# Kernel optimization log

Hardware: AMD Instinct MI355X
Metric: run time of the kernel (lower is better)

The kernel has to match this reference:

```python
import jax, jax.numpy as jnp
import numpy as np

B, N, H, D, F = 32, 128, 256, 256, 512   # batch, nodes, gru hidden, latent dim, mlp hidden
SUP = 0.5                                 # ancestor_suppression_strength
EPS = 1e-6


def _gru(x, h, Wx, Wh, bx, bh):
    """torch.nn.GRUCell math; x,h: [..., H]."""
    gx = x @ Wx + bx
    gh = h @ Wh + bh
    rx, ux, nx = jnp.split(gx, 3, axis=-1)
    rh, uh, nh = jnp.split(gh, 3, axis=-1)
    r = jax.nn.sigmoid(rx + rh)
    u = jax.nn.sigmoid(ux + uh)
    n = jnp.tanh(nx + r * nh)
    return (1.0 - u) * n + u * h


def setup_inputs() -> dict:
    key = jax.random.key(0)
    ks = jax.random.split(key, 12)
    rn = lambda k, shape, fan: jax.random.normal(k, shape, jnp.float32) * (fan ** -0.5)
    return {
        "z": jax.random.normal(ks[0], (B, D), jnp.float32),
        "targets": jax.random.randint(ks[1], (B, N, N), 0, 2, jnp.int32),
        "W_init": rn(ks[2], (D, H), D),
        "b_init": jnp.zeros((H,), jnp.float32),
        "Wx": rn(ks[3], (H, 3 * H), H),
        "Wh": rn(ks[4], (H, 3 * H), H),
        "bx": jnp.zeros((3 * H,), jnp.float32),
        "bh": jnp.zeros((3 * H,), jnp.float32),
        "W1": rn(ks[5], (2 * H + D, F), 2 * H + D),
        "b1": jnp.zeros((F,), jnp.float32),
        "W2": rn(ks[6], (F, 1), F),
        "b2": jnp.zeros((1,), jnp.float32),
    }


def reference(z, targets, W_init, b_init, Wx, Wh, bx, bh, W1, b1, W2, b2):
    # teacher-forcing link targets: strictly lower-triangular (parents have smaller index)
    tgt = jnp.tril(targets.astype(jnp.float32), k=-1)  # [B,N,N]
    idx = jnp.arange(N)

    def decode_one(z1, t1):  # z1:[D], t1:[N,N]
        h0 = jnp.tanh(z1 @ W_init + b_init)                      # decoder_init: z -> node-0 state
        states0 = jnp.zeros((N, H), jnp.float32).at[0].set(h0)
        A0 = jnp.zeros((N, N), jnp.float32)                      # ancestor bitset: A[i,j]=1 iff j ancestor of i

        def step(carry, t):
            states, A, ll = carry
            m = (idx < t).astype(jnp.float32)                    # existing-node mask
            pooled = (states * m[:, None]).sum(0) / m.sum()      # mean aggregation
            h_prov = _gru(pooled, h0, Wx, Wh, bx, bh)            # provisional new-node state
            # parent logits: MLP([h_new, h_j, z]) for every existing node j
            feat = jnp.concatenate([jnp.broadcast_to(h_prov, (N, H)), states,
                                    jnp.broadcast_to(z1, (N, D))], axis=-1)   # [N, 2H+D]
            logits = (jax.nn.relu(feat @ W1 + b1) @ W2 + b2)[:, 0]            # [N]
            row = t1[t]                                          # teacher-forced parents of node t
            anc = jnp.minimum(row @ A, 1.0)                      # j already ancestor of a chosen parent
            q = jnp.clip(jax.nn.sigmoid(logits) * (1.0 - SUP * anc), EPS, 1.0 - EPS)
            ll = ll + (m * (row * jnp.log(q) + (1.0 - row) * jnp.log1p(-q))).sum()
            A = A.at[t].set(jnp.minimum(row + row @ A, 1.0))     # ancestors(t) = parents U their ancestors
            states = states.at[t].set(h_prov)
            m2 = (idx <= t).astype(jnp.float32)[:, None]
            pooled2 = (states * m2).sum(0) / m2.sum()
            upd = _gru(jnp.broadcast_to(pooled2, (N, H)), states, Wx, Wh, bx, bh)
            states = m2 * upd + (1.0 - m2) * states              # propagate info among generated nodes
            return (states, A, ll), None

        (states, A, ll), _ = jax.lax.scan(step, (states0, A0, jnp.zeros((), jnp.float32)),
                                          jnp.arange(1, N))
        return t1, ll                                            # link matrix (teacher forced), log-likelihood

    L, ll = jax.vmap(decode_one)(z, tgt)
    return L, ll
```

## Files before the change

kernel.cpp:

```cpp
#include <hip/hip_runtime.h>
#include <hip/hip_bf16.h>
#include <math.h>

#define Bz 32
#define Nn 128
#define Hh 256
#define Dd 256
#define Ff 512
#define Gg 768
#define NT 512

typedef short v8s __attribute__((ext_vector_type(8)));
typedef float f4  __attribute__((ext_vector_type(4)));
#define MFMA(a,b,c) __builtin_amdgcn_mfma_f32_16x16x32_bf16(a,b,c,0,0,0)

#define WS_H0    0
#define WS_GH0   (WS_H0 + Bz*Hh)
#define WS_ZW1   (WS_GH0 + Bz*Gg)
#define WS_GXP   (WS_ZW1 + Bz*Ff)
#define WS_LOGP  (WS_GXP + Bz*2*8*Gg)
#define WS_BAR   (WS_LOGP + Bz*2*8*Nn)
#define WS_XS    (WS_BAR + Bz*32)
#define WS_WB    (WS_XS + Bz*32768)

#define SM_SW    0
#define SM_SST   81920
#define SM_NLDS  147456
#define SM_GXF   155648
#define SM_HPF   158720
#define SM_GX2   159232
#define SM_GHT   159616
#define SM_BASE  160000
#define SM_BHS   160256
#define SM_PSN   160640
#define SM_LOGI  160768
#define SM_TGR   161280
#define SM_RBIT  161536
#define SM_ANCW  161568
#define SM_AMASK 161600
#define SMEM_SZ  163648

__device__ __forceinline__ unsigned short f2bf(float x) {
  unsigned u = __float_as_uint(x);
  u = u + 0x7fffu + ((u >> 16) & 1u);
  return (unsigned short)(u >> 16);
}
__device__ __forceinline__ unsigned pack2(float e, float o) {
  return (unsigned)f2bf(e) | ((unsigned)f2bf(o) << 16);
}
__device__ __forceinline__ unsigned pkbf(float x, float y) {
  __hip_bfloat162 h = __float22bfloat162_rn(make_float2(x, y));
  union { __hip_bfloat162 h; unsigned u; } c; c.h = h; return c.u;
}
__device__ __forceinline__ float bf2f(unsigned short s) {
  return __uint_as_float(((unsigned)s) << 16);
}
__device__ __forceinline__ float sigm(float x) { return 1.0f / (1.0f + __expf(-x)); }
__device__ __forceinline__ float tanh_fast(float x) { return 2.0f / (1.0f + __expf(-2.0f*x)) - 1.0f; }
__device__ __forceinline__ v8s u4v(uint4 q) { union { uint4 q; v8s v; } c; c.q = q; return c.v; }

__device__ __forceinline__ void ast32(unsigned* p, unsigned v) {
  __hip_atomic_store(p, v, __ATOMIC_RELAXED, __HIP_MEMORY_SCOPE_AGENT);
}
__device__ __forceinline__ unsigned ald32(const unsigned* p) {
  return __hip_atomic_load(p, __ATOMIC_RELAXED, __HIP_MEMORY_SCOPE_AGENT);
}
__device__ __forceinline__ void ast64(unsigned long long* p, unsigned long long v) {
  __hip_atomic_store(p, v, __ATOMIC_RELAXED, __HIP_MEMORY_SCOPE_AGENT);
}
__device__ __forceinline__ unsigned long long ald64(const unsigned long long* p) {
  return __hip_atomic_load(p, __ATOMIC_RELAXED, __HIP_MEMORY_SCOPE_AGENT);
}

__device__ __forceinline__ void waitflags(const unsigned* FLG, int lane, int r, unsigned tgt)
{
  const bool watch = (lane < 8) && (lane != r);
  for (;;) {
    const unsigned f = watch ? ald32(FLG + lane) : 0xFFFFFFFFu;
    if (__ballot(f >= tgt) == 0xFFFFFFFFFFFFFFFFull) break;
  }
  __atomic_signal_fence(__ATOMIC_ACQUIRE);
}

__global__ void __launch_bounds__(256) prep_init(
    const int* __restrict__ tg, const float* __restrict__ Wx,
    const float* __restrict__ Wh, const float* __restrict__ W1,
    float* __restrict__ ws, float* __restrict__ out)
{
  const int stride = gridDim.x * blockDim.x;
  const int t0 = blockIdx.x * blockDim.x + threadIdx.x;

  for (int i = t0; i < Bz*Nn*Nn; i += stride) {
    int col = i & (Nn-1), row = (i >> 7) & (Nn-1);
    out[i] = (col < row) ? (float)tg[i] : 0.0f;
  }
  for (int i = t0; i < Bz; i += stride) out[Bz*Nn*Nn + i] = 0.0f;

  unsigned* BARu = (unsigned*)(ws + WS_BAR);
  for (int i = t0; i < Bz*32; i += stride) BARu[i] = 0u;

  unsigned* Wb = (unsigned*)(ws + WS_WB);
  for (int i = t0; i < 160*2048; i += stride) {
    int jw = i & 3, l = (i >> 2) & 63, ks = (i >> 8) & 7, nt = i >> 11;
    int k = ks*32 + (l >> 4)*8 + 2*jw;
    int n16 = l & 15;
    float lo, hi;
    if (nt < 48)       { int c = nt*16 + n16;        lo = Wh[k*Gg + c];      hi = Wh[(k+1)*Gg + c]; }
    else if (nt < 80)  { int f = (nt-48)*16 + n16;   lo = W1[(Hh+k)*Ff + f]; hi = W1[(Hh+k+1)*Ff + f]; }
    else if (nt < 128) { int c = (nt-80)*16 + n16;   lo = Wx[k*Gg + c];      hi = Wx[(k+1)*Gg + c]; }
    else               { int f = (nt-128)*16 + n16;  lo = W1[k*Ff + f];      hi = W1[(k+1)*Ff + f]; }
    Wb[i] = pack2(lo, hi);
  }
}

__global__ void __launch_bounds__(256) prep_batch(
    const float* __restrict__ z, const float* __restrict__ Wi,
    const float* __restrict__ bi, const float* __restrict__ Wh,
    const float* __restrict__ bh, const float* __restrict__ W1,
    float* __restrict__ ws)
{
  const int b = blockIdx.x, tid = threadIdx.x;
  __shared__ float zs[Dd], h0s[Hh];
  zs[tid] = z[b*Dd + tid];
  __syncthreads();
  float acc = bi[tid];
  for (int d = 0; d < Dd; ++d) acc = fmaf(zs[d], Wi[d*Hh + tid], acc);
  const float h0 = tanhf(acc);
  h0s[tid] = h0;
  ws[WS_H0 + b*Hh + tid] = h0;
  __syncthreads();
  for (int g = tid; g < Gg; g += 256) {
    float a = bh[g];
    for (int h = 0; h < Hh; ++h) a = fmaf(h0s[h], Wh[h*Gg + g], a);
    ws[WS_GH0 + b*Gg + g] = a;
  }
  for (int f = tid; f < Ff; f += 256) {
    float a = 0.0f;
    for (int d = 0; d < Dd; ++d) a = fmaf(zs[d], W1[(2*Hh + d)*Ff + f], a);
    ws[WS_ZW1 + b*Ff + f] = a;
  }
}

__device__ __forceinline__ void G_mfma(const unsigned short* SST, const uint4* SW4,
    int mt0, bool do1, int lane, f4* acc)
{
  #pragma unroll
  for (int ks = 0; ks < 8; ++ks) {
    const v8s a0 = *(const v8s*)(SST + (mt0*8 + ks)*512 + lane*8);
    const v8s w0 = u4v(SW4[(0*8 + ks)*64 + lane]);
    const v8s w1 = u4v(SW4[(1*8 + ks)*64 + lane]);
    const v8s w2 = u4v(SW4[(2*8 + ks)*64 + lane]);
    const v8s w3 = u4v(SW4[(3*8 + ks)*64 + lane]);
    const v8s w4 = u4v(SW4[(4*8 + ks)*64 + lane]);
    const v8s w5 = u4v(SW4[(5*8 + ks)*64 + lane]);
    acc[0] = MFMA(a0,w0,acc[0]); acc[1] = MFMA(a0,w1,acc[1]);
    acc[2] = MFMA(a0,w2,acc[2]); acc[3] = MFMA(a0,w3,acc[3]);
    acc[4] = MFMA(a0,w4,acc[4]); acc[5] = MFMA(a0,w5,acc[5]);
    if (do1) {
      const v8s a1 = *(const v8s*)(SST + ((mt0+1)*8 + ks)*512 + lane*8);
      acc[6]  = MFMA(a1,w0,acc[6]);  acc[7]  = MFMA(a1,w1,acc[7]);
      acc[8]  = MFMA(a1,w2,acc[8]);  acc[9]  = MFMA(a1,w3,acc[9]);
      acc[10] = MFMA(a1,w4,acc[10]); acc[11] = MFMA(a1,w5,acc[11]);
    }
  }
}

__device__ __forceinline__ void G_epi(const f4* ac, int mt, int t, int r,
    int quad, int c16, int lane, const float* GX2, const float* BHS,
    const unsigned short* SST, unsigned short* NLDS, float* PSN)
{
  #pragma unroll
  for (int ct = 0; ct < 2; ++ct) {
    const int hcl = ct*16 + c16;
    const f4 cr = ac[0 + ct], cu = ac[2 + ct], cn = ac[4 + ct];
    const float gxr = GX2[hcl], gxu = GX2[32+hcl], gxn = GX2[64+hcl];
    const float bhr = BHS[hcl], bhu = BHS[32+hcl], bhn = BHS[64+hcl];
    float colsum = 0.0f;
    #pragma unroll
    for (int rg = 0; rg < 4; ++rg) {
      const int row = mt*16 + quad*4 + rg;
      if (row < t) {
        const int spi = ((hcl>>3)*16 + quad*4 + rg)*8 + (hcl & 7);
        const float old = bf2f(SST[(mt*8 + r)*512 + spi]);
        const float rv = sigm(gxr + cr[rg] + bhr);
        const float uv = sigm(gxu + cu[rg] + bhu);
        const float nv = tanh_fast(gxn + rv*(cn[rg] + bhn));
        const float ns = (1.0f-uv)*nv + uv*old;
        NLDS[mt*512 + spi] = f2bf(ns);
        colsum += ns;
      }
    }
    colsum += __shfl_down(colsum, 16);
    colsum += __shfl_down(colsum, 32);
    if (lane < 16) atomicAdd(&PSN[ct*16 + lane], colsum);
  }
}

__device__ __forceinline__ void L_mfma(const unsigned short* SST, const uint4* SW4,
    int mt0, bool do1, int lane, f4* acc)
{
  #pragma unroll
  for (int ks = 0; ks < 8; ++ks) {
    const v8s a0 = *(const v8s*)(SST + (mt0*8 + ks)*512 + lane*8);
    const v8s c0 = u4v(SW4[(6*8 + ks)*64 + lane]);
    const v8s c1 = u4v(SW4[(7*8 + ks)*64 + lane]);
    const v8s c2 = u4v(SW4[(8*8 + ks)*64 + lane]);
    const v8s c3 = u4v(SW4[(9*8 + ks)*64 + lane]);
    acc[0] = MFMA(a0,c0,acc[0]); acc[1] = MFMA(a0,c1,acc[1]);
    acc[2] = MFMA(a0,c2,acc[2]); acc[3] = MFMA(a0,c3,acc[3]);
    if (do1) {
      const v8s a1 = *(const v8s*)(SST + ((mt0+1)*8 + ks)*512 + lane*8);
      acc[4] = MFMA(a1,c0,acc[4]); acc[5] = MFMA(a1,c1,acc[5]);
      acc[6] = MFMA(a1,c2,acc[6]); acc[7] = MFMA(a1,c3,acc[7]);
    }
  }
}

__device__ __forceinline__ void L_epi(const f4* ac, int mt, int t,
    int quad, int c16, const float* BASE, const float* w2r, float* LOGI)
{
  #pragma unroll
  for (int rg = 0; rg < 4; ++rg) {
    float v = fmaxf(ac[0][rg] + BASE[c16],    0.0f)*w2r[0]
            + fmaxf(ac[1][rg] + BASE[16+c16], 0.0f)*w2r[1]
            + fmaxf(ac[2][rg] + BASE[32+c16], 0.0f)*w2r[2]
            + fmaxf(ac[3][rg] + BASE[48+c16], 0.0f)*w2r[3];
    v += __shfl_xor(v, 1); v += __shfl_xor(v, 2);
    v += __shfl_xor(v, 4); v += __shfl_xor(v, 8);
    const int row = mt*16 + quad*4 + rg;
    if (c16 == 0 && row < t) atomicAdd(&LOGI[row], v);
  }
}

__device__ __forceinline__ void ll_gen(int tg_, int r, int lane, float b2v,
    const unsigned* LOGPb, const unsigned* RBIT, const unsigned* ANCW,
    float* out_ll)
{
  const int pp = tg_ & 1;
  const int row = 16*r + (lane >> 2);
  float term = 0.0f;
  if (row < tg_) {
    const unsigned* Lp = LOGPb + pp*1024;
    const int rr = (lane & 3)*2;
    float s = __uint_as_float(ald32(Lp + rr*128 + row))
            + __uint_as_float(ald32(Lp + (rr+1)*128 + row));
    s += __shfl_xor(s, 1); s += __shfl_xor(s, 2);
    if ((lane & 3) == 0) {
      const int w = row >> 5;
      const float anc = (float)((ANCW[pp*4 + w] >> (row & 31)) & 1u);
      float q = sigm(b2v + s) * (1.0f - 0.5f*anc);
      q = fminf(fmaxf(q, 1e-6f), 1.0f - 1e-6f);
      const unsigned rb = (RBIT[pp*4 + w] >> (row & 31)) & 1u;
      term = rb ? logf(q) : log1pf(-q);
    }
  }
  #pragma unroll
  for (int off = 1; off < 64; off <<= 1) term += __shfl_xor(term, off);
  if (lane == 0) atomicAdd(out_ll, term);
}

__global__ void __launch_bounds__(NT) decoder_main(
    const int* __restrict__ tg,
    const float* __restrict__ bx, const float* __restrict__ bh,
    const float* __restrict__ b1, const float* __restrict__ W2,
    const float* __restrict__ b2,
    float* __restrict__ ws, float* __restrict__ out)
{
  const int blk = blockIdx.x;
  const int b = blk & 31, r = blk >> 5;
  const int tid = threadIdx.x;
  const int lane = tid & 63, wv = tid >> 6;
  const int c16 = lane & 15, quad = lane >> 4;

  extern __shared__ char smem[];
  uint4* SW4 = (uint4*)(smem + SM_SW);
  unsigned short* SST = (unsigned short*)(smem + SM_SST);
  unsigned long long* SST64 = (unsigned long long*)(smem + SM_SST);
  unsigned short* NLDS = (unsigned short*)(smem + SM_NLDS);
  unsigned* NLDSu = (unsigned*)(smem + SM_NLDS);
  unsigned long long* NLDS64 = (unsigned long long*)(smem + SM_NLDS);
  float* GXF  = (float*)(smem + SM_GXF);
  unsigned short* HPF = (unsigned short*)(smem + SM_HPF);
  float* GX2  = (float*)(smem + SM_GX2);
  float* GHT  = (float*)(smem + SM_GHT);
  float* BASE = (float*)(smem + SM_BASE);
  float* BHS  = (float*)(smem + SM_BHS);
  float* PSN  = (float*)(smem + SM_PSN);
  float* LOGI = (float*)(smem + SM_LOGI);
  unsigned char* TGRu = (unsigned char*)(smem + SM_TGR);
  unsigned* RBIT  = (unsigned*)(smem + SM_RBIT);
  unsigned* ANCW  = (unsigned*)(smem + SM_ANCW);
  unsigned* AMASK = (unsigned*)(smem + SM_AMASK);

  const float* __restrict__ h0g  = ws + WS_H0  + b*Hh;
  const float* __restrict__ gh0g = ws + WS_GH0 + b*Gg;
  const float* __restrict__ zW1g = ws + WS_ZW1 + b*Ff;
  unsigned* GXPb = (unsigned*)(ws + WS_GXP) + b*2*8*Gg;
  unsigned* LOGPb = (unsigned*)(ws + WS_LOGP) + b*2*8*Nn;
  unsigned* FLG = (unsigned*)(ws + WS_BAR) + b*32;
  unsigned long long* XS64b = (unsigned long long*)(ws + WS_XS) + b*16384;
  const uint4* WB4 = (const uint4*)(ws + WS_WB);
  float* out_ll = out + Bz*Nn*Nn + b;

  for (int i = tid; i < 16384; i += NT) ((unsigned*)SST)[i] = 0u;
  for (int i = tid; i < 4096; i += NT) NLDSu[i] = 0u;
  for (int i = tid; i < 5120; i += NT) {
    const int lt = i >> 9, q = i & 511;
    int gt;
    if (lt < 6) { const int gate = lt >> 1, tt = lt & 1; gt = gate*16 + 2*r + tt; }
    else        { gt = 48 + 4*r + (lt - 6); }
    SW4[lt*512 + q] = WB4[gt*512 + q];
  }
  for (int i = tid; i < Nn*4; i += NT) AMASK[i] = 0u;
  if (tid < 96) BHS[tid] = bh[(tid >> 5)*256 + 32*r + (tid & 31)];
  if (tid < 128) TGRu[128 + tid] = (unsigned char)tg[b*Nn*Nn + 1*Nn + tid];
  float w2r[4];
  #pragma unroll
  for (int ft = 0; ft < 4; ++ft) w2r[ft] = W2[64*r + ft*16 + c16];
  const float b2v = b2[0];
  float p_bx[3][4], p_gh[3][4], p_h0[4];
  #pragma unroll
  for (int k = 0; k < 4; ++k) {
    const int c = 4*lane + k;
    p_h0[k] = h0g[c];
    #pragma unroll
    for (int g3 = 0; g3 < 3; ++g3) {
      p_bx[g3][k] = bx[g3*256 + c];
      p_gh[g3][k] = gh0g[g3*256 + c];
    }
  }
  int colj[2]; float auxj[2];
  #pragma unroll
  for (int jj = 0; jj < 2; ++jj) {
    const int j = 2*wv + jj;
    colj[jj] = 0; auxj[jj] = 0.0f;
    if (j >= 6 && j < 12) {
      const int jx = j - 6, g = jx >> 1, tt = jx & 1;
      const int col = g*256 + 32*r + tt*16 + c16;
      colj[jj] = col; auxj[jj] = bx[col];
    } else if (j >= 12) {
      const int ft = j - 12, f = 64*r + ft*16 + c16;
      auxj[jj] = zW1g[f] + b1[f];
    }
  }
  __syncthreads();
  if (tid < Hh) {
    const int c = tid;
    SST[(c>>5)*512 + ((c>>3)&3)*128 + (c&7)] = f2bf(h0g[c]);
  }
  if (tid < 32) PSN[tid] = h0g[32*r + tid];
  __syncthreads();
  {
    union { unsigned u[4]; v8s v; } cv;
    const float4 a0 = *(const float4*)(PSN + quad*8);
    const float4 a1 = *(const float4*)(PSN + quad*8 + 4);
    cv.u[0] = pkbf(a0.x, a0.y); cv.u[1] = pkbf(a0.z, a0.w);
    cv.u[2] = pkbf(a1.x, a1.y); cv.u[3] = pkbf(a1.z, a1.w);
    const v8s avp = cv.v;
    unsigned* GXPw = GXPb + 1*8*Gg + r*Gg;
    #pragma unroll
    for (int k2 = 0; k2 < 6; ++k2) {
      const int nt = wv*6 + k2;
      f4 c = {0.0f,0.0f,0.0f,0.0f};
      c = MFMA(avp, u4v(WB4[(80 + nt)*512 + r*64 + lane]), c);
      if (quad == 0) ast32(GXPw + nt*16 + c16, __float_as_uint(c[0]));
    }
  }
  if (tid < 128) ast64(XS64b + r*128 + tid, SST64[r*128 + tid]);
  __builtin_amdgcn_s_waitcnt(0x0F70);
  __syncthreads();
  if (tid == 0) { __atomic_signal_fence(__ATOMIC_RELEASE); ast32(FLG + r, 1u); }

  for (int t = 1; t < Nn; ++t) {
    const int tp = t & 1;
    const float invt  = 1.0f / (float)t;
    const float invt1 = 1.0f / (float)(t + 1);
    const int Mr   = (t + 15) >> 4;
    const int Mtot = (t + 16) >> 4;
    const int mtc  = t >> 4;
    const int nG = (Mr + 1) >> 1, nL = (Mr + 1) >> 1;
    const int njobs = nG + nL;

    waitflags(FLG, lane, r, (unsigned)t);

    if (tid < 384) {
      const unsigned long long* GXPr = (const unsigned long long*)(GXPb + tp*8*Gg);
      unsigned long long g[8];
      #pragma unroll
      for (int rr = 0; rr < 8; ++rr) g[rr] = ald64(GXPr + rr*384 + tid);
      float s0 = 0.0f, s1 = 0.0f;
      #pragma unroll
      for (int rr = 0; rr < 8; ++rr) {
        s0 += __uint_as_float((unsigned)g[rr]);
        s1 += __uint_as_float((unsigned)(g[rr] >> 32));
      }
      GXF[2*tid]   = s0;
      GXF[2*tid+1] = s1;
    }
    if (tid < 448) {
      const unsigned long long* XSr = XS64b + ((t-1)&1)*8192;
      for (int i = tid; i < Mr*1024; i += 448) {
        if (((i >> 7) & 7) != r) SST64[i] = ald64(XSr + i);
      }
    }
    if (wv == 6) {
      const int v0 = TGRu[tp*128 + lane];
      const int v1 = TGRu[tp*128 + lane + 64];
      const unsigned long long bal0 = __ballot(lane < t && v0);
      const unsigned long long bal1 = __ballot((lane + 64) < t && v1);
      if (lane == 0) {
        RBIT[tp*4+0] = (unsigned)bal0; RBIT[tp*4+1] = (unsigned)(bal0 >> 32);
        RBIT[tp*4+2] = (unsigned)bal1; RBIT[tp*4+3] = (unsigned)(bal1 >> 32);
      }
      LOGI[lane] = 0.0f; LOGI[lane+64] = 0.0f;
      if (lane < 32) PSN[lane] = 0.0f;
      unsigned m0=0,m1=0,m2=0,m3=0;
      if (lane < t && v0) {
        m0 = AMASK[lane*4+0]; m1 = AMASK[lane*4+1];
        m2 = AMASK[lane*4+2]; m3 = AMASK[lane*4+3];
      }
      if (lane + 64 < t && v1) {
        m0 |= AMASK[(lane+64)*4+0]; m1 |= AMASK[(lane+64)*4+1];
        m2 |= AMASK[(lane+64)*4+2]; m3 |= AMASK[(lane+64)*4+3];
      }
      #pragma unroll
      for (int off = 1; off < 64; off <<= 1) {
        m0 |= __shfl_xor(m0, off); m1 |= __shfl_xor(m1, off);
        m2 |= __shfl_xor(m2, off); m3 |= __shfl_xor(m3, off);
      }
      if (lane == 0) {
        ANCW[tp*4+0] = m0; ANCW[tp*4+1] = m1;
        ANCW[tp*4+2] = m2; ANCW[tp*4+3] = m3;
      }
    }
    if (wv == 7 && t > 1) ll_gen(t-1, r, lane, b2v, LOGPb, RBIT, ANCW, out_ll);
    __syncthreads();

    {
      float hp[4];
      const float* gr = GXF + 4*lane;
      #pragma unroll
      for (int k = 0; k < 4; ++k) {
        const float rv = sigm(gr[k]*invt       + p_bx[0][k] + p_gh[0][k]);
        const float uv = sigm(gr[256+k]*invt   + p_bx[1][k] + p_gh[1][k]);
        const float nv = tanh_fast(gr[512+k]*invt + p_bx[2][k] + rv*p_gh[2][k]);
        hp[k] = (1.0f - uv)*nv + uv*p_h0[k];
      }
      uint2 pk;
      pk.x = pack2(hp[0], hp[1]); pk.y = pack2(hp[2], hp[3]);
      *(uint2*)(HPF + 4*lane) = pk;
      if (wv == 0 && lane < 4)
        AMASK[t*4 + lane] = RBIT[tp*4 + lane] | ANCW[tp*4 + lane];
      if (wv == 1 && (t & 15) == 0) {
        for (int q = lane; q < 256; q += 64) NLDSu[mtc*256 + q] = 0u;
      }
      v8s av[8];
      #pragma unroll
      for (int ks = 0; ks < 8; ++ks) av[ks] = *(const v8s*)(HPF + ks*32 + quad*8);
      #pragma unroll
      for (int jj = 0; jj < 2; ++jj) {
        const int j = 2*wv + jj;
        f4 c = {0.0f,0.0f,0.0f,0.0f};
        if (j < 6) {
          #pragma unroll
          for (int ks = 0; ks < 8; ++ks) c = MFMA(av[ks], u4v(SW4[(j*8 + ks)*64 + lane]), c);
          if (quad == 0) GHT[(j>>1)*32 + (j&1)*16 + c16] = c[0];
        } else if (j < 12) {
          const int jx = j - 6, g = jx >> 1, tt = jx & 1;
          const uint4* Bp = WB4 + (80 + g*16 + 2*r + tt)*512 + lane;
          #pragma unroll
          for (int ks = 0; ks < 8; ++ks) c = MFMA(av[ks], u4v(Bp[ks*64]), c);
          if (quad == 0) GX2[g*32 + tt*16 + c16] = (c[0] + GXF[colj[jj]])*invt1 + auxj[jj];
        } else {
          const int ft = j - 12;
          const uint4* Bp = WB4 + (128 + 4*r + ft)*512 + lane;
          #pragma unroll
          for (int ks = 0; ks < 8; ++ks) c = MFMA(av[ks], u4v(Bp[ks*64]), c);
          if (quad == 0) BASE[ft*16 + c16] = c[0] + auxj[jj];
        }
      }
    }
    __syncthreads();

    if (wv < njobs) {
      if (wv < nG) {
        const int mt0 = 2*wv;
        const bool do1 = (mt0 + 1 < Mr);
        f4 acc[12];
        #pragma unroll
        for (int i = 0; i < 12; ++i) acc[i] = (f4){0.0f,0.0f,0.0f,0.0f};
        G_mfma(SST, SW4, mt0, do1, lane, acc);
        G_epi(acc, mt0, t, r, quad, c16, lane, GX2, BHS, SST, NLDS, PSN);
        if (do1) G_epi(acc+6, mt0+1, t, r, quad, c16, lane, GX2, BHS, SST, NLDS, PSN);
      } else {
        const int mt0 = 2*(wv - nG);
        const bool do1 = (mt0 + 1 < Mr);
        f4 acc[8];
        #pragma unroll
        for (int i = 0; i < 8; ++i) acc[i] = (f4){0.0f,0.0f,0.0f,0.0f};
        L_mfma(SST, SW4, mt0, do1, lane, acc);
        L_epi(acc, mt0, t, quad, c16, BASE, w2r, LOGI);
        if (do1) L_epi(acc+4, mt0+1, t, quad, c16, BASE, w2r, LOGI);
      }
    }
    if (wv == 7 && lane < 32) {
      const int hcl = lane;
      const float rv = sigm(GX2[hcl]    + GHT[hcl]    + BHS[hcl]);
      const float uv = sigm(GX2[32+hcl] + GHT[32+hcl] + BHS[32+hcl]);
      const float nv = tanh_fast(GX2[64+hcl] + rv*(GHT[64+hcl] + BHS[64+hcl]));
      const float old = bf2f(HPF[32*r + hcl]);
      const float ns = (1.0f - uv)*nv + uv*old;
      const int spi = ((hcl>>3)*16 + (t & 15))*8 + (hcl & 7);
      NLDS[mtc*512 + spi] = f2bf(ns);
      atomicAdd(&PSN[hcl], ns);
    }
    __syncthreads();

    {
      union { unsigned u[4]; v8s v; } cv;
      const float4 a0 = *(const float4*)(PSN + quad*8);
      const float4 a1 = *(const float4*)(PSN + quad*8 + 4);
      cv.u[0] = pkbf(a0.x, a0.y); cv.u[1] = pkbf(a0.z, a0.w);
      cv.u[2] = pkbf(a1.x, a1.y); cv.u[3] = pkbf(a1.z, a1.w);
      const v8s avp = cv.v;
      unsigned* GXPw = GXPb + ((t+1)&1)*8*Gg + r*Gg;
      #pragma unroll
      for (int k2 = 0; k2 < 6; ++k2) {
        const int nt = wv*6 + k2;
        f4 c = {0.0f,0.0f,0.0f,0.0f};
        c = MFMA(avp, u4v(WB4[(80 + nt)*512 + r*64 + lane]), c);
        if (quad == 0) ast32(GXPw + nt*16 + c16, __float_as_uint(c[0]));
      }
    }
    {
      unsigned long long* XSw = XS64b + tp*8192;
      for (int i = tid; i < Mtot*128; i += NT) {
        const int mt = i >> 7, q = i & 127;
        const unsigned long long v = NLDS64[i];
        ast64(XSw + (mt*8 + r)*128 + q, v);
        SST64[(mt*8 + r)*128 + q] = v;
      }
    }
    if (tid < 64)
      ast64((unsigned long long*)LOGPb + tp*512 + r*64 + tid,
            ((const unsigned long long*)LOGI)[tid]);
    if (wv == 7 && t + 1 < Nn) {
      const int base = b*Nn*Nn + (t+1)*Nn;
      TGRu[((t+1)&1)*128 + lane]      = (unsigned char)tg[base + lane];
      TGRu[((t+1)&1)*128 + lane + 64] = (unsigned char)tg[base + lane + 64];
    }
    __builtin_amdgcn_s_waitcnt(0x0F70);
    __syncthreads();
    if (tid == 0) { __atomic_signal_fence(__ATOMIC_RELEASE); ast32(FLG + r, (unsigned)(t + 1)); }
  }

  if (wv == 7) {
    waitflags(FLG, lane, r, (unsigned)Nn);
    ll_gen(Nn - 1, r, lane, b2v, LOGPb, RBIT, ANCW, out_ll);
  }
}

extern "C" void kernel_launch(void* const* d_in, const int* in_sizes, int n_in,
                              void* d_out, int out_size, void* d_ws, size_t ws_size,
                              hipStream_t stream)
{
  const float* z  = (const float*)d_in[0];
  const int*   tg = (const int*)  d_in[1];
  const float* Wi = (const float*)d_in[2];
  const float* bi = (const float*)d_in[3];
  const float* Wx = (const float*)d_in[4];
  const float* Wh = (const float*)d_in[5];
  const float* bx = (const float*)d_in[6];
  const float* bh = (const float*)d_in[7];
  const float* W1 = (const float*)d_in[8];
  const float* b1 = (const float*)d_in[9];
  const float* W2 = (const float*)d_in[10];
  const float* b2 = (const float*)d_in[11];
  float* out = (float*)d_out;
  float* ws  = (float*)d_ws;

  hipFuncSetAttribute((const void*)decoder_main,
                      hipFuncAttributeMaxDynamicSharedMemorySize, SMEM_SZ);

  hipLaunchKernelGGL(prep_init, dim3(512), dim3(256), 0, stream, tg, Wx, Wh, W1, ws, out);
  hipLaunchKernelGGL(prep_batch, dim3(Bz), dim3(256), 0, stream, z, Wi, bi, Wh, bh, W1, ws);

  void* args[] = { (void*)&tg, (void*)&bx, (void*)&bh, (void*)&b1,
                   (void*)&W2, (void*)&b2, (void*)&ws, (void*)&out };
  hipLaunchCooperativeKernel((void*)decoder_main, dim3(256), dim3(NT),
                             args, SMEM_SZ, stream);
}
```

Baseline: 2.341 ms.

## Read neighbor states directly from global exchange and overlap provisional GRU with MFMA

Drops the shared-memory copy of all peer blocks' node states (SST) and has the G/L MFMA wavefronts load their A operands straight from the global exchange buffer. The per-step flag polling is replaced by a counter-based barrier across the 8 cooperating blocks. Waves 0-5 start the big GEMMs while waves 6-7 compute the provisional-node GRU, the gx reduction and the ancestor bits, which removes one __syncthreads phase per step and shrinks LDS use. The risk is higher-latency global loads on the critical MFMA path and a shared-counter barrier that may cost more than the flag scheme.

```diff
diff --git a/kernel.cpp b/kernel.cpp
--- a/kernel.cpp
+++ b/kernel.cpp
@@ -24,21 +24,20 @@
 #define WS_WB    (WS_XS + Bz*32768)
 
 #define SM_SW    0
-#define SM_SST   81920
-#define SM_NLDS  147456
-#define SM_GXF   155648
-#define SM_HPF   158720
-#define SM_GX2   159232
-#define SM_GHT   159616
-#define SM_BASE  160000
-#define SM_BHS   160256
-#define SM_PSN   160640
-#define SM_LOGI  160768
-#define SM_TGR   161280
-#define SM_RBIT  161536
-#define SM_ANCW  161568
-#define SM_AMASK 161600
-#define SMEM_SZ  163648
+#define SM_NL    81920
+#define SM_GXF   98304
+#define SM_HPF   101376
+#define SM_GX2   101888
+#define SM_GHT   102272
+#define SM_BASE  102656
+#define SM_BHS   102912
+#define SM_PSN   103296
+#define SM_LOGI  103424
+#define SM_TGR   103936
+#define SM_RBIT  104192
+#define SM_ANCW  104224
+#define SM_AMASK 104256
+#define SMEM_SZ  106304
 
 __device__ __forceinline__ unsigned short f2bf(float x) {
   unsigned u = __float_as_uint(x);
@@ -72,14 +71,17 @@
   return __hip_atomic_load(p, __ATOMIC_RELAXED, __HIP_MEMORY_SCOPE_AGENT);
 }
 
-__device__ __forceinline__ void waitflags(const unsigned* FLG, int lane, int r, unsigned tgt)
-{
-  const bool watch = (lane < 8) && (lane != r);
-  for (;;) {
-    const unsigned f = watch ? ald32(FLG + lane) : 0xFFFFFFFFu;
-    if (__ballot(f >= tgt) == 0xFFFFFFFFFFFFFFFFull) break;
-  }
-  __atomic_signal_fence(__ATOMIC_ACQUIRE);
+__device__ __forceinline__ void bbar(unsigned* cnt, unsigned& seq)
+{
+  __builtin_amdgcn_s_waitcnt(0x0F70);
+  __syncthreads();
+  seq += 8;
+  if (threadIdx.x == 0) {
+    __hip_atomic_fetch_add(cnt, 1u, __ATOMIC_RELAXED, __HIP_MEMORY_SCOPE_AGENT);
+    while (__hip_atomic_load(cnt, __ATOMIC_RELAXED, __HIP_MEMORY_SCOPE_AGENT) < seq)
+      __builtin_amdgcn_s_sleep(1);
+  }
+  __syncthreads();
 }
 
 __global__ void __launch_bounds__(256) prep_init(
@@ -141,33 +143,45 @@
   }
 }
 
-__device__ __forceinline__ void G_mfma(const unsigned short* SST, const uint4* SW4,
+__device__ __forceinline__ v8s ldA(const unsigned long long* XSr, int mt, int ks, int lane)
+{
+  const unsigned long long* p = XSr + (mt*8 + ks)*128 + lane*2;
+  union { unsigned long long q[2]; v8s v; } c;
+  c.q[0] = ald64(p); c.q[1] = ald64(p + 1);
+  return c.v;
+}
+
+__device__ __forceinline__ void G_mfma(const unsigned long long* XSr, const uint4* SW4,
     int mt0, bool do1, int lane, f4* acc)
 {
+  v8s a0f[8], a1f[8];
   #pragma unroll
   for (int ks = 0; ks < 8; ++ks) {
-    const v8s a0 = *(const v8s*)(SST + (mt0*8 + ks)*512 + lane*8);
+    a0f[ks] = ldA(XSr, mt0, ks, lane);
+    if (do1) a1f[ks] = ldA(XSr, mt0 + 1, ks, lane);
+  }
+  #pragma unroll
+  for (int ks = 0; ks < 8; ++ks) {
     const v8s w0 = u4v(SW4[(0*8 + ks)*64 + lane]);
     const v8s w1 = u4v(SW4[(1*8 + ks)*64 + lane]);
     const v8s w2 = u4v(SW4[(2*8 + ks)*64 + lane]);
     const v8s w3 = u4v(SW4[(3*8 + ks)*64 + lane]);
     const v8s w4 = u4v(SW4[(4*8 + ks)*64 + lane]);
     const v8s w5 = u4v(SW4[(5*8 + ks)*64 + lane]);
-    acc[0] = MFMA(a0,w0,acc[0]); acc[1] = MFMA(a0,w1,acc[1]);
-    acc[2] = MFMA(a0,w2,acc[2]); acc[3] = MFMA(a0,w3,acc[3]);
-    acc[4] = MFMA(a0,w4,acc[4]); acc[5] = MFMA(a0,w5,acc[5]);
+    acc[0] = MFMA(a0f[ks],w0,acc[0]); acc[1] = MFMA(a0f[ks],w1,acc[1]);
+    acc[2] = MFMA(a0f[ks],w2,acc[2]); acc[3] = MFMA(a0f[ks],w3,acc[3]);
+    acc[4] = MFMA(a0f[ks],w4,acc[4]); acc[5] = MFMA(a0f[ks],w5,acc[5]);
     if (do1) {
-      const v8s a1 = *(const v8s*)(SST + ((mt0+1)*8 + ks)*512 + lane*8);
-      acc[6]  = MFMA(a1,w0,acc[6]);  acc[7]  = MFMA(a1,w1,acc[7]);
-      acc[8]  = MFMA(a1,w2,acc[8]);  acc[9]  = MFMA(a1,w3,acc[9]);
-      acc[10] = MFMA(a1,w4,acc[10]); acc[11] = MFMA(a1,w5,acc[11]);
-    }
-  }
-}
-
-__device__ __forceinline__ void G_epi(const f4* ac, int mt, int t, int r,
+      acc[6]  = MFMA(a1f[ks],w0,acc[6]);  acc[7]  = MFMA(a1f[ks],w1,acc[7]);
+      acc[8]  = MFMA(a1f[ks],w2,acc[8]);  acc[9]  = MFMA(a1f[ks],w3,acc[9]);
+      acc[10] = MFMA(a1f[ks],w4,acc[10]); acc[11] = MFMA(a1f[ks],w5,acc[11]);
+    }
+  }
+}
+
+__device__ __forceinline__ void G_epi(const f4* ac, int mt, int t,
     int quad, int c16, int lane, const float* GX2, const float* BHS,
-    const unsigned short* SST, unsigned short* NLDS, float* PSN)
+    const unsigned short* NLo, unsigned short* NLn, float* PSN)
 {
   #pragma unroll
   for (int ct = 0; ct < 2; ++ct) {
@@ -181,12 +195,12 @@
       const int row = mt*16 + quad*4 + rg;
       if (row < t) {
         const int spi = ((hcl>>3)*16 + quad*4 + rg)*8 + (hcl & 7);
-        const float old = bf2f(SST[(mt*8 + r)*512 + spi]);
+        const float old = bf2f(NLo[mt*512 + spi]);
         const float rv = sigm(gxr + cr[rg] + bhr);
         const float uv = sigm(gxu + cu[rg] + bhu);
         const float nv = tanh_fast(gxn + rv*(cn[rg] + bhn));
         const float ns = (1.0f-uv)*nv + uv*old;
-        NLDS[mt*512 + spi] = f2bf(ns);
+        NLn[mt*512 + spi] = f2bf(ns);
         colsum += ns;
       }
     }
@@ -196,22 +210,26 @@
   }
 }
 
-__device__ __forceinline__ void L_mfma(const unsigned short* SST, const uint4* SW4,
+__device__ __forceinline__ void L_mfma(const unsigned long long* XSr, const uint4* SW4,
     int mt0, bool do1, int lane, f4* acc)
 {
+  v8s a0f[8], a1f[8];
   #pragma unroll
   for (int ks = 0; ks < 8; ++ks) {
-    const v8s a0 = *(const v8s*)(SST + (mt0*8 + ks)*512 + lane*8);
+    a0f[ks] = ldA(XSr, mt0, ks, lane);
+    if (do1) a1f[ks] = ldA(XSr, mt0 + 1, ks, lane);
+  }
+  #pragma unroll
+  for (int ks = 0; ks < 8; ++ks) {
     const v8s c0 = u4v(SW4[(6*8 + ks)*64 + lane]);
     const v8s c1 = u4v(SW4[(7*8 + ks)*64 + lane]);
     const v8s c2 = u4v(SW4[(8*8 + ks)*64 + lane]);
     const v8s c3 = u4v(SW4[(9*8 + ks)*64 + lane]);
-    acc[0] = MFMA(a0,c0,acc[0]); acc[1] = MFMA(a0,c1,acc[1]);
-    acc[2] = MFMA(a0,c2,acc[2]); acc[3] = MFMA(a0,c3,acc[3]);
+    acc[0] = MFMA(a0f[ks],c0,acc[0]); acc[1] = MFMA(a0f[ks],c1,acc[1]);
+    acc[2] = MFMA(a0f[ks],c2,acc[2]); acc[3] = MFMA(a0f[ks],c3,acc[3]);
     if (do1) {
-      const v8s a1 = *(const v8s*)(SST + ((mt0+1)*8 + ks)*512 + lane*8);
-      acc[4] = MFMA(a1,c0,acc[4]); acc[5] = MFMA(a1,c1,acc[5]);
-      acc[6] = MFMA(a1,c2,acc[6]); acc[7] = MFMA(a1,c3,acc[7]);
+      acc[4] = MFMA(a1f[ks],c0,acc[4]); acc[5] = MFMA(a1f[ks],c1,acc[5]);
+      acc[6] = MFMA(a1f[ks],c2,acc[6]); acc[7] = MFMA(a1f[ks],c3,acc[7]);
     }
   }
 }
@@ -274,11 +292,8 @@
 
   extern __shared__ char smem[];
   uint4* SW4 = (uint4*)(smem + SM_SW);
-  unsigned short* SST = (unsigned short*)(smem + SM_SST);
-  unsigned long long* SST64 = (unsigned long long*)(smem + SM_SST);
-  unsigned short* NLDS = (unsigned short*)(smem + SM_NLDS);
-  unsigned* NLDSu = (unsigned*)(smem + SM_NLDS);
-  unsigned long long* NLDS64 = (unsigned long long*)(smem + SM_NLDS);
+  unsigned short* NLb = (unsigned short*)(smem + SM_NL);
+  unsigned* NLu = (unsigned*)(smem + SM_NL);
   float* GXF  = (float*)(smem + SM_GXF);
   unsigned short* HPF = (unsigned short*)(smem + SM_HPF);
   float* GX2  = (float*)(smem + SM_GX2);
@@ -297,13 +312,12 @@
   const float* __restrict__ zW1g = ws + WS_ZW1 + b*Ff;
   unsigned* GXPb = (unsigned*)(ws + WS_GXP) + b*2*8*Gg;
   unsigned* LOGPb = (unsigned*)(ws + WS_LOGP) + b*2*8*Nn;
-  unsigned* FLG = (unsigned*)(ws + WS_BAR) + b*32;
+  unsigned* bar = (unsigned*)(ws + WS_BAR) + b*32;
   unsigned long long* XS64b = (unsigned long long*)(ws + WS_XS) + b*16384;
   const uint4* WB4 = (const uint4*)(ws + WS_WB);
   float* out_ll = out + Bz*Nn*Nn + b;
 
-  for (int i = tid; i < 16384; i += NT) ((unsigned*)SST)[i] = 0u;
-  for (int i = tid; i < 4096; i += NT) NLDSu[i] = 0u;
+  for (int i = tid; i < 4096; i += NT) NLu[i] = 0u;
   for (int i = tid; i < 5120; i += NT) {
     const int lt = i >> 9, q = i & 511;
     int gt;
@@ -319,36 +333,39 @@
   for (int ft = 0; ft < 4; ++ft) w2r[ft] = W2[64*r + ft*16 + c16];
   const float b2v = b2[0];
   float p_bx[3][4], p_gh[3][4], p_h0[4];
-  #pragma unroll
-  for (int k = 0; k < 4; ++k) {
-    const int c = 4*lane + k;
-    p_h0[k] = h0g[c];
+  int colj[8]; float auxj[8];
+  if (wv >= 6) {
     #pragma unroll
-    for (int g3 = 0; g3 < 3; ++g3) {
-      p_bx[g3][k] = bx[g3*256 + c];
-      p_gh[g3][k] = gh0g[g3*256 + c];
-    }
-  }
-  int colj[2]; float auxj[2];
-  #pragma unroll
-  for (int jj = 0; jj < 2; ++jj) {
-    const int j = 2*wv + jj;
-    colj[jj] = 0; auxj[jj] = 0.0f;
-    if (j >= 6 && j < 12) {
-      const int jx = j - 6, g = jx >> 1, tt = jx & 1;
-      const int col = g*256 + 32*r + tt*16 + c16;
-      colj[jj] = col; auxj[jj] = bx[col];
-    } else if (j >= 12) {
-      const int ft = j - 12, f = 64*r + ft*16 + c16;
-      auxj[jj] = zW1g[f] + b1[f];
-    }
-  }
+    for (int k = 0; k < 4; ++k) {
+      const int c = 4*lane + k;
+      p_h0[k] = h0g[c];
+      #pragma unroll
+      for (int g3 = 0; g3 < 3; ++g3) {
+        p_bx[g3][k] = bx[g3*256 + c];
+        p_gh[g3][k] = gh0g[g3*256 + c];
+      }
+    }
+    #pragma unroll
+    for (int jj = 0; jj < 8; ++jj) {
+      const int j = 2*jj + (wv - 6);
+      colj[jj] = 0; auxj[jj] = 0.0f;
+      if (j >= 6 && j < 12) {
+        const int jx = j - 6, g = jx >> 1, tt = jx & 1;
+        const int col = g*256 + 32*r + tt*16 + c16;
+        colj[jj] = col; auxj[jj] = bx[col];
+      } else if (j >= 12) {
+        const int ft = j - 12, f = 64*r + ft*16 + c16;
+        auxj[jj] = zW1g[f] + b1[f];
+      }
+    }
+  }
+  unsigned bseq = 0;
   __syncthreads();
-  if (tid < Hh) {
-    const int c = tid;
-    SST[(c>>5)*512 + ((c>>3)&3)*128 + (c&7)] = f2bf(h0g[c]);
-  }
-  if (tid < 32) PSN[tid] = h0g[32*r + tid];
+  if (tid < 32) {
+    const int hcl = tid;
+    NLb[(hcl>>3)*128 + (hcl&7)] = f2bf(h0g[32*r + hcl]);
+    PSN[hcl] = h0g[32*r + hcl];
+  }
   __syncthreads();
   {
     union { unsigned u[4]; v8s v; } cv;
@@ -366,10 +383,8 @@
       if (quad == 0) ast32(GXPw + nt*16 + c16, __float_as_uint(c[0]));
     }
   }
-  if (tid < 128) ast64(XS64b + r*128 + tid, SST64[r*128 + tid]);
-  __builtin_amdgcn_s_waitcnt(0x0F70);
-  __syncthreads();
-  if (tid == 0) { __atomic_signal_fence(__ATOMIC_RELEASE); ast32(FLG + r, 1u); }
+  if (tid < 128) ast64(XS64b + r*128 + tid, ((const unsigned long long*)NLb)[tid]);
+  bbar(bar, bseq);
 
   for (int t = 1; t < Nn; ++t) {
     const int tp = t & 1;
@@ -378,141 +393,152 @@
     const int Mr   = (t + 15) >> 4;
     const int Mtot = (t + 16) >> 4;
     const int mtc  = t >> 4;
-    const int nG = (Mr + 1) >> 1, nL = (Mr + 1) >> 1;
-    const int njobs = nG + nL;
-
-    waitflags(FLG, lane, r, (unsigned)t);
-
-    if (tid < 384) {
-      const unsigned long long* GXPr = (const unsigned long long*)(GXPb + tp*8*Gg);
-      unsigned long long g[8];
-      #pragma unroll
-      for (int rr = 0; rr < 8; ++rr) g[rr] = ald64(GXPr + rr*384 + tid);
-      float s0 = 0.0f, s1 = 0.0f;
-      #pragma unroll
-      for (int rr = 0; rr < 8; ++rr) {
-        s0 += __uint_as_float((unsigned)g[rr]);
-        s1 += __uint_as_float((unsigned)(g[rr] >> 32));
-      }
-      GXF[2*tid]   = s0;
-      GXF[2*tid+1] = s1;
-    }
-    if (tid < 448) {
-      const unsigned long long* XSr = XS64b + ((t-1)&1)*8192;
-      for (int i = tid; i < Mr*1024; i += 448) {
-        if (((i >> 7) & 7) != r) SST64[i] = ald64(XSr + i);
-      }
-    }
-    if (wv == 6) {
-      const int v0 = TGRu[tp*128 + lane];
-      const int v1 = TGRu[tp*128 + lane + 64];
-      const unsigned long long bal0 = __ballot(lane < t && v0);
-      const unsigned long long bal1 = __ballot((lane + 64) < t && v1);
-      if (lane == 0) {
-        RBIT[tp*4+0] = (unsigned)bal0; RBIT[tp*4+1] = (unsigned)(bal0 >> 32);
-        RBIT[tp*4+2] = (unsigned)bal1; RBIT[tp*4+3] = (unsigned)(bal1 >> 32);
-      }
-      LOGI[lane] = 0.0f; LOGI[lane+64] = 0.0f;
-      if (lane < 32) PSN[lane] = 0.0f;
-      unsigned m0=0,m1=0,m2=0,m3=0;
-      if (lane < t && v0) {
-        m0 = AMASK[lane*4+0]; m1 = AMASK[lane*4+1];
-        m2 = AMASK[lane*4+2]; m3 = AMASK[lane*4+3];
-      }
-      if (lane + 64 < t && v1) {
-        m0 |= AMASK[(lane+64)*4+0]; m1 |= AMASK[(lane+64)*4+1];
-        m2 |= AMASK[(lane+64)*4+2]; m3 |= AMASK[(lane+64)*4+3];
-      }
-      #pragma unroll
-      for (int off = 1; off < 64; off <<= 1) {
-        m0 |= __shfl_xor(m0, off); m1 |= __shfl_xor(m1, off);
-        m2 |= __shfl_xor(m2, off); m3 |= __shfl_xor(m3, off);
-      }
-      if (lane == 0) {
-        ANCW[tp*4+0] = m0; ANCW[tp*4+1] = m1;
-        ANCW[tp*4+2] = m2; ANCW[tp*4+3] = m3;
-      }
-    }
-    if (wv == 7 && t > 1) ll_gen(t-1, r, lane, b2v, LOGPb, RBIT, ANCW, out_ll);
+    const int nG = (Mr + 1) >> 1;
+    const int njobs = 2*nG;
+    const unsigned long long* XSr = XS64b + (1-tp)*8192;
+    unsigned long long* XSw = XS64b + tp*8192;
+    const unsigned short* NLo = NLb + (1-tp)*4096;
+    unsigned short* NLn = NLb + tp*4096;
+
+    f4 acc[12];
+    #pragma unroll
+    for (int i = 0; i < 12; ++i) acc[i] = (f4){0.0f,0.0f,0.0f,0.0f};
+    int kindA = 0, mtA = 0; bool haveA = false, d1A = false;
+    if (wv < 6) {
+      if (wv < njobs) {
+        haveA = true;
+        if (wv < nG) { kindA = 0; mtA = 2*wv; }
+        else         { kindA = 1; mtA = 2*(wv - nG); }
+        d1A = (mtA + 1 < Mr);
+        if (kindA == 0) G_mfma(XSr, SW4, mtA, d1A, lane, acc);
+        else            L_mfma(XSr, SW4, mtA, d1A, lane, acc);
+      }
+    } else {
+      if (wv == 6) {
+        const int v0 = TGRu[tp*128 + lane];
+        const int v1 = TGRu[tp*128 + 64 + lane];
+        const unsigned long long bal0 = __ballot(lane < t && v0);
+        const unsigned long long bal1 = __ballot((lane + 64) < t && v1);
+        unsigned m0=0,m1=0,m2=0,m3=0;
+        if (lane < t && v0) {
+          m0 = AMASK[lane*4+0]; m1 = AMASK[lane*4+1];
+          m2 = AMASK[lane*4+2]; m3 = AMASK[lane*4+3];
+        }
+        if (lane + 64 < t && v1) {
+          m0 |= AMASK[(lane+64)*4+0]; m1 |= AMASK[(lane+64)*4+1];
+          m2 |= AMASK[(lane+64)*4+2]; m3 |= AMASK[(lane+64)*4+3];
+        }
+        #pragma unroll
+        for (int off = 1; off < 64; off <<= 1) {
+          m0 |= __shfl_xor(m0, off); m1 |= __shfl_xor(m1, off);
+          m2 |= __shfl_xor(m2, off); m3 |= __shfl_xor(m3, off);
+        }
+        LOGI[lane] = 0.0f; LOGI[lane + 64] = 0.0f;
+        if (lane < 32) PSN[lane] = 0.0f;
+        if (lane < 4) {
+          const unsigned rbw = (lane == 0) ? (unsigned)bal0 :
+                               (lane == 1) ? (unsigned)(bal0 >> 32) :
+                               (lane == 2) ? (unsigned)bal1 : (unsigned)(bal1 >> 32);
+          const unsigned anw = (lane == 0) ? m0 : (lane == 1) ? m1 : (lane == 2) ? m2 : m3;
+          RBIT[tp*4 + lane] = rbw;
+          ANCW[tp*4 + lane] = anw;
+          AMASK[t*4 + lane] = rbw | anw;
+        }
+      }
+      {
+        const unsigned long long* GXPr = (const unsigned long long*)(GXPb + tp*8*Gg);
+        #pragma unroll
+        for (int g = 0; g < 6; ++g) {
+          const int col = g*64 + lane;
+          unsigned long long v[8];
+          #pragma unroll
+          for (int rr = 0; rr < 8; ++rr) v[rr] = ald64(GXPr + rr*384 + col);
+          float s0 = 0.0f, s1 = 0.0f;
+          #pragma unroll
+          for (int rr = 0; rr < 8; ++rr) {
+            s0 += __uint_as_float((unsigned)v[rr]);
+            s1 += __uint_as_float((unsigned)(v[rr] >> 32));
+          }
+          GXF[2*col] = s0; GXF[2*col + 1] = s1;
+        }
+      }
+      {
+        float hp[4];
+        #pragma unroll
+        for (int k = 0; k < 4; ++k) {
+          const int c = 4*lane + k;
+          const float rv = sigm(GXF[c]*invt       + p_bx[0][k] + p_gh[0][k]);
+          const float uv = sigm(GXF[256+c]*invt   + p_bx[1][k] + p_gh[1][k]);
+          const float nv = tanh_fast(GXF[512+c]*invt + p_bx[2][k] + rv*p_gh[2][k]);
+          hp[k] = (1.0f - uv)*nv + uv*p_h0[k];
+        }
+        uint2 pk;
+        pk.x = pack2(hp[0], hp[1]); pk.y = pack2(hp[2], hp[3]);
+        *(uint2*)(HPF + 4*lane) = pk;
+      }
+      {
+        v8s av[8];
+        #pragma unroll
+        for (int ks = 0; ks < 8; ++ks) av[ks] = *(const v8s*)(HPF + ks*32 + quad*8);
+        #pragma unroll
+        for (int jj = 0; jj < 8; ++jj) {
+          const int j = 2*jj + (wv - 6);
+          f4 c = {0.0f,0.0f,0.0f,0.0f};
+          if (j < 6) {
+            #pragma unroll
+            for (int ks = 0; ks < 8; ++ks) c = MFMA(av[ks], u4v(SW4[(j*8 + ks)*64 + lane]), c);
+            if (quad == 0) GHT[(j>>1)*32 + (j&1)*16 + c16] = c[0];
+          } else if (j < 12) {
+            const int jx = j - 6, g = jx >> 1, tt = jx & 1;
+            const uint4* Bp = WB4 + (80 + g*16 + 2*r + tt)*512 + lane;
+            #pragma unroll
+            for (int ks = 0; ks < 8; ++ks) c = MFMA(av[ks], u4v(Bp[ks*64]), c);
+            if (quad == 0) GX2[g*32 + tt*16 + c16] = (c[0] + GXF[colj[jj]])*invt1 + auxj[jj];
+          } else {
+            const int ft = j - 12;
+            const uint4* Bp = WB4 + (128 + 4*r + ft)*512 + lane;
+            #pragma unroll
+            for (int ks = 0; ks < 8; ++ks) c = MFMA(av[ks], u4v(Bp[ks*64]), c);
+            if (quad == 0) BASE[ft*16 + c16] = c[0] + auxj[jj];
+          }
+        }
+      }
+    }
     __syncthreads();
 
-    {
-      float hp[4];
-      const float* gr = GXF + 4*lane;
-      #pragma unroll
-      for (int k = 0; k < 4; ++k) {
-        const float rv = sigm(gr[k]*invt       + p_bx[0][k] + p_gh[0][k]);
-        const float uv = sigm(gr[256+k]*invt   + p_bx[1][k] + p_gh[1][k]);
-        const float nv = tanh_fast(gr[512+k]*invt + p_bx[2][k] + rv*p_gh[2][k]);
-        hp[k] = (1.0f - uv)*nv + uv*p_h0[k];
-      }
-      uint2 pk;
-      pk.x = pack2(hp[0], hp[1]); pk.y = pack2(hp[2], hp[3]);
-      *(uint2*)(HPF + 4*lane) = pk;
-      if (wv == 0 && lane < 4)
-        AMASK[t*4 + lane] = RBIT[tp*4 + lane] | ANCW[tp*4 + lane];
-      if (wv == 1 && (t & 15) == 0) {
-        for (int q = lane; q < 256; q += 64) NLDSu[mtc*256 + q] = 0u;
-      }
-      v8s av[8];
-      #pragma unroll
-      for (int ks = 0; ks < 8; ++ks) av[ks] = *(const v8s*)(HPF + ks*32 + quad*8);
-      #pragma unroll
-      for (int jj = 0; jj < 2; ++jj) {
-        const int j = 2*wv + jj;
-        f4 c = {0.0f,0.0f,0.0f,0.0f};
-        if (j < 6) {
-          #pragma unroll
-          for (int ks = 0; ks < 8; ++ks) c = MFMA(av[ks], u4v(SW4[(j*8 + ks)*64 + lane]), c);
-          if (quad == 0) GHT[(j>>1)*32 + (j&1)*16 + c16] = c[0];
-        } else if (j < 12) {
-          const int jx = j - 6, g = jx >> 1, tt = jx & 1;
-          const uint4* Bp = WB4 + (80 + g*16 + 2*r + tt)*512 + lane;
-          #pragma unroll
-          for (int ks = 0; ks < 8; ++ks) c = MFMA(av[ks], u4v(Bp[ks*64]), c);
-          if (quad == 0) GX2[g*32 + tt*16 + c16] = (c[0] + GXF[colj[jj]])*invt1 + auxj[jj];
+    if (wv < 6) {
+      if (haveA) {
+        if (kindA == 0) {
+          G_epi(acc,     mtA,   t, quad, c16, lane, GX2, BHS, NLo, NLn, PSN);
+          if (d1A) G_epi(acc+6, mtA+1, t, quad, c16, lane, GX2, BHS, NLo, NLn, PSN);
         } else {
-          const int ft = j - 12;
-          const uint4* Bp = WB4 + (128 + 4*r + ft)*512 + lane;
-          #pragma unroll
-          for (int ks = 0; ks < 8; ++ks) c = MFMA(av[ks], u4v(Bp[ks*64]), c);
-          if (quad == 0) BASE[ft*16 + c16] = c[0] + auxj[jj];
-        }
-      }
-    }
-    __syncthreads();
-
-    if (wv < njobs) {
-      if (wv < nG) {
-        const int mt0 = 2*wv;
-        const bool do1 = (mt0 + 1 < Mr);
-        f4 acc[12];
+          L_epi(acc,     mtA,   t, quad, c16, BASE, w2r, LOGI);
+          if (d1A) L_epi(acc+4, mtA+1, t, quad, c16, BASE, w2r, LOGI);
+        }
+      }
+    } else {
+      if (wv == 7 && lane < 32) {
+        const int hcl = lane;
+        const float rv = sigm(GX2[hcl]    + GHT[hcl]    + BHS[hcl]);
+        const float uv = sigm(GX2[32+hcl] + GHT[32+hcl] + BHS[32+hcl]);
+        const float nv = tanh_fast(GX2[64+hcl] + rv*(GHT[64+hcl] + BHS[64+hcl]));
+        const float old = bf2f(HPF[32*r + hcl]);
+        const float ns = (1.0f - uv)*nv + uv*old;
+        const int spi = ((hcl>>3)*16 + (t & 15))*8 + (hcl & 7);
+        NLn[mtc*512 + spi] = f2bf(ns);
+        atomicAdd(&PSN[hcl], ns);
+      }
+      if (njobs == 8) {
+        const int jB = wv;
+        const int mtB = 2*(jB - nG);
+        const bool d1B = (mtB + 1 < Mr);
+        f4 acc2[8];
         #pragma unroll
-        for (int i = 0; i < 12; ++i) acc[i] = (f4){0.0f,0.0f,0.0f,0.0f};
-        G_mfma(SST, SW4, mt0, do1, lane, acc);
-        G_epi(acc, mt0, t, r, quad, c16, lane, GX2, BHS, SST, NLDS, PSN);
-        if (do1) G_epi(acc+6, mt0+1, t, r, quad, c16, lane, GX2, BHS, SST, NLDS, PSN);
-      } else {
-        const int mt0 = 2*(wv - nG);
-        const bool do1 = (mt0 + 1 < Mr);
-        f4 acc[8];
-        #pragma unroll
-        for (int i = 0; i < 8; ++i) acc[i] = (f4){0.0f,0.0f,0.0f,0.0f};
-        L_mfma(SST, SW4, mt0, do1, lane, acc);
-        L_epi(acc, mt0, t, quad, c16, BASE, w2r, LOGI);
-        if (do1) L_epi(acc+4, mt0+1, t, quad, c16, BASE, w2r, LOGI);
-      }
-    }
-    if (wv == 7 && lane < 32) {
-      const int hcl = lane;
-      const float rv = sigm(GX2[hcl]    + GHT[hcl]    + BHS[hcl]);
-      const float uv = sigm(GX2[32+hcl] + GHT[32+hcl] + BHS[32+hcl]);
-      const float nv = tanh_fast(GX2[64+hcl] + rv*(GHT[64+hcl] + BHS[64+hcl]));
-      const float old = bf2f(HPF[32*r + hcl]);
-      const float ns = (1.0f - uv)*nv + uv*old;
-      const int spi = ((hcl>>3)*16 + (t & 15))*8 + (hcl & 7);
-      NLDS[mtc*512 + spi] = f2bf(ns);
-      atomicAdd(&PSN[hcl], ns);
+        for (int i = 0; i < 8; ++i) acc2[i] = (f4){0.0f,0.0f,0.0f,0.0f};
+        L_mfma(XSr, SW4, mtB, d1B, lane, acc2);
+        L_epi(acc2,     mtB,   t, quad, c16, BASE, w2r, LOGI);
+        if (d1B) L_epi(acc2+4, mtB+1, t, quad, c16, BASE, w2r, LOGI);
+      }
     }
     __syncthreads();
 
@@ -533,31 +559,25 @@
       }
     }
     {
-      unsigned long long* XSw = XS64b + tp*8192;
+      const unsigned long long* NLn64 = (const unsigned long long*)NLn;
       for (int i = tid; i < Mtot*128; i += NT) {
         const int mt = i >> 7, q = i & 127;
-        const unsigned long long v = NLDS64[i];
-        ast64(XSw + (mt*8 + r)*128 + q, v);
-        SST64[(mt*8 + r)*128 + q] = v;
+        ast64(XSw + (mt*8 + r)*128 + q, NLn64[i]);
       }
     }
     if (tid < 64)
       ast64((unsigned long long*)LOGPb + tp*512 + r*64 + tid,
             ((const unsigned long long*)LOGI)[tid]);
-    if (wv == 7 && t + 1 < Nn) {
+    if (wv == 6 && t + 1 < Nn) {
       const int base = b*Nn*Nn + (t+1)*Nn;
       TGRu[((t+1)&1)*128 + lane]      = (unsigned char)tg[base + lane];
       TGRu[((t+1)&1)*128 + lane + 64] = (unsigned char)tg[base + lane + 64];
     }
-    __builtin_amdgcn_s_waitcnt(0x0F70);
-    __syncthreads();
-    if (tid == 0) { __atomic_signal_fence(__ATOMIC_RELEASE); ast32(FLG + r, (unsigned)(t + 1)); }
-  }
-
-  if (wv == 7) {
-    waitflags(FLG, lane, r, (unsigned)Nn);
-    ll_gen(Nn - 1, r, lane, b2v, LOGPb, RBIT, ANCW, out_ll);
-  }
+    if (wv == 7 && t > 1) ll_gen(t-1, r, lane, b2v, LOGPb, RBIT, ANCW, out_ll);
+    bbar(bar, bseq);
+  }
+
+  if (wv == 7) ll_gen(Nn - 1, r, lane, b2v, LOGPb, RBIT, ANCW, out_ll);
 }
 
 extern "C" void kernel_launch(void* const* d_in, const int* in_sizes, int n_in,
```

Measured after the change: 2.839 ms. +21.3%, slower.
